# Kernel tuning notes

Measured on AMD Instinct MI355X. Metric: run time of the kernel, lower is better.

## Reference

```python
import jax, jax.numpy as jnp
import numpy as np

B, S, D = 2, 4096, 768
H = 12
HD = D // H  # 64


def setup_inputs() -> dict:
    key = jax.random.key(0)
    ks = jax.random.split(key, 5)
    scale = 1.0 / np.sqrt(D)
    x = jax.random.normal(ks[0], (B, S, D), dtype=jnp.float32)
    Wq = jax.random.normal(ks[1], (D, D), dtype=jnp.float32) * scale
    Wk = jax.random.normal(ks[2], (D, D), dtype=jnp.float32) * scale
    Wv = jax.random.normal(ks[3], (D, D), dtype=jnp.float32) * scale
    Wo = jax.random.normal(ks[4], (D, D), dtype=jnp.float32) * scale
    zb = jnp.zeros((D,), dtype=jnp.float32)
    return {"x": x, "Wq": Wq, "bq": zb, "Wk": Wk, "bk": zb, "Wv": Wv, "bv": zb, "Wo": Wo, "bo": zb}


def reference(x, Wq, bq, Wk, bk, Wv, bv, Wo, bo):
    b, s, d = x.shape
    # projections: nn.Linear computes x @ W^T + b; here W is stored as [in, out]-style [D, D]
    def proj(W, bias):
        y = jnp.einsum('bsd,ed->bse', x, W) + bias  # matches torch Linear (weight [out,in])
        return y.reshape(b, s, H, HD).transpose(0, 2, 1, 3)  # [B,H,S,HD]
    q = proj(Wq, bq)
    k = proj(Wk, bk)
    v = proj(Wv, bv)
    att = jnp.einsum('bhqd,bhkd->bhqk', q, k) / np.sqrt(HD).astype(np.float32)
    causal = jnp.tril(jnp.ones((s, s), dtype=bool))
    att = jnp.where(causal, att, -jnp.inf)
    att = jax.nn.softmax(att, axis=-1)  # dropout p=0 (eval)
    y = jnp.einsum('bhqk,bhkd->bhqd', att, v)
    y = y.transpose(0, 2, 1, 3).reshape(b, s, d)
    return jnp.einsum('bsd,ed->bse', y, Wo) + bo
```

## Files before the change

### kernel.cpp

```cpp
#include <hip/hip_runtime.h>
#include <hip/hip_bf16.h>

typedef __bf16 bf16;
typedef __attribute__((ext_vector_type(8))) __bf16 bf16x8;
typedef __attribute__((ext_vector_type(4))) __bf16 bf16x4;
typedef __attribute__((ext_vector_type(4))) float f32x4;
typedef __attribute__((ext_vector_type(16))) float f32x16;

#if __has_builtin(__builtin_amdgcn_permlane32_swap)
#define HAVE_PLSWAP 1
typedef __attribute__((ext_vector_type(2))) unsigned uint2v;
#endif

#define MFMA16(a, b, c) __builtin_amdgcn_mfma_f32_16x16x32_bf16((a), (b), (c), 0, 0, 0)
#define MFMA32(a, b, c) __builtin_amdgcn_mfma_f32_32x32x16_bf16((a), (b), (c), 0, 0, 0)

__device__ __forceinline__ void gload_lds16(const bf16* g, bf16* l) {
  __builtin_amdgcn_global_load_lds(
      (const __attribute__((address_space(1))) void*)g,
      (__attribute__((address_space(3))) void*)l, 16, 0, 0);
}

__device__ __forceinline__ unsigned pkbf(float a, float b) {
  union { unsigned u; bf16 h[2]; } w;
  w.h[0] = (bf16)a; w.h[1] = (bf16)b;
  return w.u;
}

#define CBAR(N)                                               \
  do {                                                        \
    asm volatile("s_waitcnt vmcnt(" #N ") lgkmcnt(0)" ::: "memory"); \
    __builtin_amdgcn_s_barrier();                             \
    __builtin_amdgcn_sched_barrier(0);                        \
  } while (0)

__global__ void cvt_all(const float* __restrict__ x,
                        const float* __restrict__ wq, const float* __restrict__ wk,
                        const float* __restrict__ wv, const float* __restrict__ wo,
                        bf16* __restrict__ xb, bf16* __restrict__ Wb) {
  constexpr int NX4 = 6291456 / 4;
  constexpr int NW4 = 589824 / 4;
  constexpr int TOT = NX4 + 4 * NW4;
  int stride = gridDim.x * blockDim.x;
  for (int i = blockIdx.x * blockDim.x + threadIdx.x; i < TOT; i += stride) {
    const float4* src;
    bf16x4* dst;
    if (i < NX4) {
      src = reinterpret_cast<const float4*>(x) + i;
      dst = reinterpret_cast<bf16x4*>(xb) + i;
    } else {
      int j = i - NX4;
      int w = j / NW4, r = j - w * NW4;
      const float* sp = (w == 0) ? wq : (w == 1) ? wk : (w == 2) ? wv : wo;
      src = reinterpret_cast<const float4*>(sp) + r;
      dst = reinterpret_cast<bf16x4*>(Wb) + j;
    }
    float4 v = *src;
    bf16x4 o = {(bf16)v.x, (bf16)v.y, (bf16)v.z, (bf16)v.w};
    *dst = o;
  }
}

template <bool OUT_BF16>
__global__ __launch_bounds__(256) void gemm_bt(
    const bf16* __restrict__ A, const bf16* __restrict__ W,
    const float* __restrict__ b0, const float* __restrict__ b1, const float* __restrict__ b2,
    float* __restrict__ Cf, bf16* __restrict__ Cb,
    int M, int N, int K) {
  const int z = blockIdx.z;
  const bf16* Wz = W + (size_t)z * N * K;
  const float* bias = (z == 0) ? b0 : (z == 1 ? b1 : b2);

  __shared__ alignas(16) bf16 As[128 * 64];
  __shared__ alignas(16) bf16 Bs[128 * 64];

  const int tid = threadIdx.x;
  const int wave = tid >> 6, lane = tid & 63;
  const int lr = lane & 15, lg = lane >> 4;
  const int wr = wave >> 1, wc = wave & 1;
  const int m0 = blockIdx.y * 128, n0 = blockIdx.x * 128;

  f32x4 acc[4][4] = {};

  for (int k0 = 0; k0 < K; k0 += 64) {
    __syncthreads();
#pragma unroll
    for (int j = 0; j < 4; ++j) {
      int cb = j * 256 + wave * 64;
      int c = cb + lane;
      int row = c >> 3, x = c & 7;
      int xs = x ^ (row & 7);
      gload_lds16(&A[(size_t)(m0 + row) * K + k0 + xs * 8], &As[cb * 8]);
      gload_lds16(&Wz[(size_t)(n0 + row) * K + k0 + xs * 8], &Bs[cb * 8]);
    }
    __syncthreads();
#pragma unroll
    for (int kk = 0; kk < 2; ++kk) {
      bf16x8 af[4], bfr[4];
#pragma unroll
      for (int m = 0; m < 4; ++m) {
        int row = wr * 64 + m * 16 + lr;
        int ch = (kk * 4 + lg) ^ (row & 7);
        af[m] = *reinterpret_cast<const bf16x8*>(&As[row * 64 + ch * 8]);
      }
#pragma unroll
      for (int n = 0; n < 4; ++n) {
        int row = wc * 64 + n * 16 + lr;
        int ch = (kk * 4 + lg) ^ (row & 7);
        bfr[n] = *reinterpret_cast<const bf16x8*>(&Bs[row * 64 + ch * 8]);
      }
      __builtin_amdgcn_s_setprio(1);
#pragma unroll
      for (int m = 0; m < 4; ++m)
#pragma unroll
        for (int n = 0; n < 4; ++n)
          acc[m][n] = MFMA16(af[m], bfr[n], acc[m][n]);
      __builtin_amdgcn_s_setprio(0);
    }
  }

#pragma unroll
  for (int m = 0; m < 4; ++m) {
#pragma unroll
    for (int n = 0; n < 4; ++n) {
#pragma unroll
      for (int i = 0; i < 4; ++i) {
        int row = m0 + wr * 64 + m * 16 + lg * 4 + i;
        int col = n0 + wc * 64 + n * 16 + lr;
        float v = acc[m][n][i] + bias[col];
        if constexpr (OUT_BF16)
          (Cb + (size_t)z * M * N)[(size_t)row * N + col] = (bf16)v;
        else
          Cf[(size_t)row * N + col] = v;
      }
    }
  }
}

__global__ __launch_bounds__(256, 3) void attn32(
    const bf16* __restrict__ Q, const bf16* __restrict__ K,
    const bf16* __restrict__ V, bf16* __restrict__ Y) {
  constexpr int S = 4096, D = 768;
  const int lin = blockIdx.x;
  const int xcd = lin & 7, idx = lin >> 3;
  const int seg = idx >> 5;
  const int pair = xcd * 3 + seg;
  const int jj = idx & 31;
  const int qb = (seg == 0) ? jj
               : (seg == 1) ? ((jj + 16) & 31)
               : (jj < 16 ? 30 - 2 * jj : 63 - 2 * jj);
  const int h = pair % 12, bb = pair / 12;

  const int tid = threadIdx.x, wave = tid >> 6, lane = tid & 63;
  const int ln = lane & 31, hi = lane >> 5;

  const int qw0 = qb * 128 + wave * 32;
  const int qrow = qw0 + ln;
  const int nt = 2 * qb + 2;

  __shared__ alignas(16) bf16 Ks[3][64 * 64];
  __shared__ alignas(16) bf16 Vt[2][64 * 64];

  const size_t head = (size_t)bb * S * D + (size_t)h * 64;
  const float SC2 = 0.125f * 1.44269504089f;

  union U32x4 { unsigned u[4]; bf16x8 v; };
  U32x4 onesU;
  onesU.u[0] = onesU.u[1] = onesU.u[2] = onesU.u[3] = 0x3F803F80u;
  const bf16x8 onesf = onesU.v;

  const f32x16 z16 = {};

  bf16x8 qf[4];
  {
    const bf16* qp = Q + head + (size_t)qrow * D;
#pragma unroll
    for (int c = 0; c < 4; ++c) {
      bf16x8 tq = *reinterpret_cast<const bf16x8*>(qp + c * 16 + hi * 8);
#pragma unroll
      for (int e = 0; e < 8; ++e) tq[e] = (bf16)((float)tq[e] * SC2);
      qf[c] = tq;
    }
  }

  int fOff[4];
#pragma unroll
  for (int i = 0; i < 4; ++i)
    fOff[i] = ln * 64 + ((((2 * i + hi) ^ ln) & 7) * 8);

  const bf16* gk[2];
  int ldsK[2];
#pragma unroll
  for (int j2 = 0; j2 < 2; ++j2) {
    int c = j2 * 256 + tid;
    int r = c >> 3, ch = c & 7;
    gk[j2] = K + head + (size_t)r * D + ((ch ^ (r & 7)) & 7) * 8;
    ldsK[j2] = (j2 * 256 + wave * 64) * 8;
  }

  const int k0v = (tid & 31) * 2, d0 = (tid >> 5) * 8;
  const bf16* gv0 = V + head + (size_t)k0v * D + d0;
  const bf16* gv1 = gv0 + D;
  int wOff[8];
#pragma unroll
  for (int e = 0; e < 8; ++e)
    wOff[e] = (d0 + e) * 64 + ((((k0v >> 3) ^ e) & 7) * 8) + (k0v & 7);

  f32x16 accO0 = {}, accO1 = {}, accL = {};

  auto stageK = [&](int buf) {
#pragma unroll
    for (int j2 = 0; j2 < 2; ++j2) {
      gload_lds16(gk[j2], &Ks[buf][ldsK[j2]]);
      gk[j2] += 64 * D;
    }
  };
  auto loadV = [&](bf16x8* vv) {
    vv[0] = *reinterpret_cast<const bf16x8*>(gv0);
    vv[1] = *reinterpret_cast<const bf16x8*>(gv1);
    gv0 += 64 * D;
    gv1 += 64 * D;
  };
  auto writeV = [&](const bf16x8* vv, int buf) {
#pragma unroll
    for (int e = 0; e < 8; ++e) {
      union { unsigned u; bf16 h[2]; } pw;
      pw.h[0] = vv[0][e]; pw.h[1] = vv[1][e];
      *reinterpret_cast<unsigned*>(&Vt[buf][wOff[e]]) = pw.u;
    }
  };

  {
    bf16x8 v0[2];
    loadV(v0);
    stageK(0);
    stageK(1);
    writeV(v0, 0);
  }
  CBAR(2);

  int curV = 0, curK = 0, sK = 2;
  for (int t = 0; t < nt; ++t) {
    const int kv0 = t * 64;
    const bool more = (t + 1 < nt);
    bf16x8 vnext[2];
    if (more) {
      loadV(vnext);
      if (t + 2 < nt) { stageK(sK); sK = (sK == 2) ? 0 : sK + 1; }
    }

    if (kv0 <= qw0 + 31) {
      const bf16* ksp = &Ks[curK][0];
      f32x16 s0, s1;
      __builtin_amdgcn_s_setprio(1);
      {
        bf16x8 kf0 = *reinterpret_cast<const bf16x8*>(ksp + fOff[0]);
        bf16x8 kf1 = *reinterpret_cast<const bf16x8*>(ksp + fOff[0] + 2048);
        s0 = MFMA32(kf0, qf[0], z16);
        s1 = MFMA32(kf1, qf[0], z16);
      }
#pragma unroll
      for (int c = 1; c < 4; ++c) {
        bf16x8 kf0 = *reinterpret_cast<const bf16x8*>(ksp + fOff[c]);
        bf16x8 kf1 = *reinterpret_cast<const bf16x8*>(ksp + fOff[c] + 2048);
        s0 = MFMA32(kf0, qf[c], s0);
        s1 = MFMA32(kf1, qf[c], s1);
      }
      __builtin_amdgcn_s_setprio(0);

      if (kv0 + 63 > qw0) {
#pragma unroll
        for (int r = 0; r < 16; ++r) {
          int kl = (r & 3) + 8 * (r >> 2) + 4 * hi;
          if (kv0 + kl > qrow) s0[r] = -1e30f;
          if (kv0 + 32 + kl > qrow) s1[r] = -1e30f;
        }
      }

      float p[32];
#pragma unroll
      for (int r = 0; r < 16; ++r) {
        p[r] = __builtin_amdgcn_exp2f(s0[r]);
        p[16 + r] = __builtin_amdgcn_exp2f(s1[r]);
      }

      const bf16* vtp = &Vt[curV][0];
      __builtin_amdgcn_s_setprio(1);
#pragma unroll
      for (int kg = 0; kg < 2; ++kg) {
        const float* pv = &p[kg * 16];
        unsigned w0 = pkbf(pv[0], pv[1]), w1 = pkbf(pv[2], pv[3]);
        unsigned w2 = pkbf(pv[4], pv[5]), w3 = pkbf(pv[6], pv[7]);
        unsigned w4 = pkbf(pv[8], pv[9]), w5 = pkbf(pv[10], pv[11]);
        unsigned w6 = pkbf(pv[12], pv[13]), w7 = pkbf(pv[14], pv[15]);
        union { unsigned u[4]; bf16x8 v; } fe, fo;
#if HAVE_PLSWAP
        uint2v r02 = __builtin_amdgcn_permlane32_swap(w0, w2, false, false);
        uint2v r13 = __builtin_amdgcn_permlane32_swap(w1, w3, false, false);
        uint2v r46 = __builtin_amdgcn_permlane32_swap(w4, w6, false, false);
        uint2v r57 = __builtin_amdgcn_permlane32_swap(w5, w7, false, false);
        fe.u[0] = r02.x; fe.u[1] = r13.x; fe.u[2] = r02.y; fe.u[3] = r13.y;
        fo.u[0] = r46.x; fo.u[1] = r57.x; fo.u[2] = r46.y; fo.u[3] = r57.y;
#else
        unsigned X0 = hi ? w0 : w2, X1 = hi ? w1 : w3;
        unsigned X2 = hi ? w4 : w6, X3 = hi ? w5 : w7;
        unsigned Y0 = __shfl_xor((int)X0, 32), Y1 = __shfl_xor((int)X1, 32);
        unsigned Y2 = __shfl_xor((int)X2, 32), Y3 = __shfl_xor((int)X3, 32);
        fe.u[0] = hi ? Y0 : w0; fe.u[1] = hi ? Y1 : w1;
        fe.u[2] = hi ? w2 : Y0; fe.u[3] = hi ? w3 : Y1;
        fo.u[0] = hi ? Y2 : w4; fo.u[1] = hi ? Y3 : w5;
        fo.u[2] = hi ? w6 : Y2; fo.u[3] = hi ? w7 : Y3;
#endif
#pragma unroll
        for (int half = 0; half < 2; ++half) {
          int kc = 2 * kg + half;
          bf16x8 pf = half ? fo.v : fe.v;
          bf16x8 vf0 = *reinterpret_cast<const bf16x8*>(vtp + fOff[kc]);
          bf16x8 vf1 = *reinterpret_cast<const bf16x8*>(vtp + fOff[kc] + 2048);
          accO0 = MFMA32(vf0, pf, accO0);
          accO1 = MFMA32(vf1, pf, accO1);
          accL = MFMA32(onesf, pf, accL);
        }
      }
      __builtin_amdgcn_s_setprio(0);
    }

    if (more) {
      writeV(vnext, curV ^ 1);
      CBAR(2);
      curV ^= 1;
      curK = (curK == 2) ? 0 : curK + 1;
    }
  }

  float inv = 1.f / accL[0];
  bf16* yp = Y + head + (size_t)qrow * D;
#pragma unroll
  for (int g = 0; g < 4; ++g) {
    bf16x4 o0, o1;
#pragma unroll
    for (int i = 0; i < 4; ++i) {
      o0[i] = (bf16)(accO0[g * 4 + i] * inv);
      o1[i] = (bf16)(accO1[g * 4 + i] * inv);
    }
    *reinterpret_cast<bf16x4*>(yp + 8 * g + 4 * hi) = o0;
    *reinterpret_cast<bf16x4*>(yp + 32 + 8 * g + 4 * hi) = o1;
  }
}

extern "C" void kernel_launch(void* const* d_in, const int* in_sizes, int n_in,
                              void* d_out, int out_size, void* d_ws, size_t ws_size,
                              hipStream_t stream) {
  const float* x  = (const float*)d_in[0];
  const float* Wq = (const float*)d_in[1];
  const float* bq = (const float*)d_in[2];
  const float* Wk = (const float*)d_in[3];
  const float* bk = (const float*)d_in[4];
  const float* Wv = (const float*)d_in[5];
  const float* bv = (const float*)d_in[6];
  const float* Wo = (const float*)d_in[7];
  const float* bo = (const float*)d_in[8];
  float* out = (float*)d_out;

  constexpr int Bx = 2, S = 4096, Dd = 768;
  constexpr int M = Bx * S;
  constexpr size_t XB = (size_t)M * Dd;
  constexpr size_t WB = (size_t)Dd * Dd;

  char* ws = (char*)d_ws;
  bf16* xb = (bf16*)ws;
  bf16* Wb = (bf16*)(ws + 2 * XB);
  bf16* Qb = (bf16*)(ws + 2 * XB + 8 * WB);
  bf16* Kb = Qb + XB;
  bf16* Vb = Kb + XB;
  bf16* Yb = Vb + XB;

  cvt_all<<<2048, 256, 0, stream>>>(x, Wq, Wk, Wv, Wo, xb, Wb);

  gemm_bt<true><<<dim3(6, 64, 3), 256, 0, stream>>>(
      xb, Wb, bq, bk, bv, nullptr, Qb, M, Dd, Dd);

  attn32<<<dim3(768), 256, 0, stream>>>(Qb, Kb, Vb, Yb);

  gemm_bt<false><<<dim3(6, 64, 1), 256, 0, stream>>>(
      Yb, Wb + 3 * WB, bo, bo, bo, out, nullptr, M, Dd, Dd);
}
```

Measured before the change: 177.2 us.

## Split causal attention KV range in two halves and merge with combine kernel

```diff
diff --git a/kernel.cpp b/kernel.cpp
--- a/kernel.cpp
+++ b/kernel.cpp
@@ -137,15 +137,19 @@
   }
 }
 
-__global__ __launch_bounds__(256, 3) void attn32(
+__global__ __launch_bounds__(256, 4) void attn32(
     const bf16* __restrict__ Q, const bf16* __restrict__ K,
-    const bf16* __restrict__ V, bf16* __restrict__ Y) {
+    const bf16* __restrict__ V,
+    bf16* __restrict__ Oa, bf16* __restrict__ Ob,
+    float* __restrict__ La, float* __restrict__ Lb) {
   constexpr int S = 4096, D = 768;
   const int lin = blockIdx.x;
   const int xcd = lin & 7, idx = lin >> 3;
-  const int seg = idx >> 5;
+  const int seg = idx >> 6;
   const int pair = xcd * 3 + seg;
-  const int jj = idx & 31;
+  const int rem = idx & 63;
+  const int jj = rem >> 1;
+  const int part = rem & 1;
   const int qb = (seg == 0) ? jj
                : (seg == 1) ? ((jj + 16) & 31)
                : (jj < 16 ? 30 - 2 * jj : 63 - 2 * jj);
@@ -156,7 +160,8 @@
 
   const int qw0 = qb * 128 + wave * 32;
   const int qrow = qw0 + ln;
-  const int nt = 2 * qb + 2;
+  const int ntL = qb + 1;
+  const int t0rows = part * ntL * 64;
 
   __shared__ alignas(16) bf16 Ks[3][64 * 64];
   __shared__ alignas(16) bf16 Vt[2][64 * 64];
@@ -194,12 +199,12 @@
   for (int j2 = 0; j2 < 2; ++j2) {
     int c = j2 * 256 + tid;
     int r = c >> 3, ch = c & 7;
-    gk[j2] = K + head + (size_t)r * D + ((ch ^ (r & 7)) & 7) * 8;
+    gk[j2] = K + head + (size_t)(r + t0rows) * D + ((ch ^ (r & 7)) & 7) * 8;
     ldsK[j2] = (j2 * 256 + wave * 64) * 8;
   }
 
   const int k0v = (tid & 31) * 2, d0 = (tid >> 5) * 8;
-  const bf16* gv0 = V + head + (size_t)k0v * D + d0;
+  const bf16* gv0 = V + head + (size_t)(k0v + t0rows) * D + d0;
   const bf16* gv1 = gv0 + D;
   int wOff[8];
 #pragma unroll
@@ -240,13 +245,13 @@
   CBAR(2);
 
   int curV = 0, curK = 0, sK = 2;
-  for (int t = 0; t < nt; ++t) {
-    const int kv0 = t * 64;
-    const bool more = (t + 1 < nt);
+  for (int t = 0; t < ntL; ++t) {
+    const int kv0 = (part * ntL + t) * 64;
+    const bool more = (t + 1 < ntL);
     bf16x8 vnext[2];
     if (more) {
       loadV(vnext);
-      if (t + 2 < nt) { stageK(sK); sK = (sK == 2) ? 0 : sK + 1; }
+      if (t + 2 < ntL) { stageK(sK); sK = (sK == 2) ? 0 : sK + 1; }
     }
 
     if (kv0 <= qw0 + 31) {
@@ -333,19 +338,40 @@
     }
   }
 
-  float inv = 1.f / accL[0];
-  bf16* yp = Y + head + (size_t)qrow * D;
+  bf16* op = (part ? Ob : Oa) + head + (size_t)qrow * D;
 #pragma unroll
   for (int g = 0; g < 4; ++g) {
     bf16x4 o0, o1;
 #pragma unroll
     for (int i = 0; i < 4; ++i) {
-      o0[i] = (bf16)(accO0[g * 4 + i] * inv);
-      o1[i] = (bf16)(accO1[g * 4 + i] * inv);
-    }
-    *reinterpret_cast<bf16x4*>(yp + 8 * g + 4 * hi) = o0;
-    *reinterpret_cast<bf16x4*>(yp + 32 + 8 * g + 4 * hi) = o1;
-  }
+      o0[i] = (bf16)accO0[g * 4 + i];
+      o1[i] = (bf16)accO1[g * 4 + i];
+    }
+    *reinterpret_cast<bf16x4*>(op + 8 * g + 4 * hi) = o0;
+    *reinterpret_cast<bf16x4*>(op + 32 + 8 * g + 4 * hi) = o1;
+  }
+  (part ? Lb : La)[((bb * 12 + h) << 12) + qrow] = accL[0];
+}
+
+__global__ __launch_bounds__(256) void combine(
+    const bf16* __restrict__ Oa, const bf16* __restrict__ Ob,
+    const float* __restrict__ La, const float* __restrict__ Lb,
+    bf16* __restrict__ Y) {
+  int i = blockIdx.x * blockDim.x + threadIdx.x;
+  if (i >= 786432) return;
+  int e = i * 8;
+  int rowlin = e >> 6;
+  int h = rowlin % 12;
+  int t = rowlin / 12;
+  int s = t & 4095, bb = t >> 12;
+  int lidx = ((bb * 12 + h) << 12) + s;
+  float inv = 1.f / (La[lidx] + Lb[lidx]);
+  bf16x8 a = *reinterpret_cast<const bf16x8*>(Oa + e);
+  bf16x8 b = *reinterpret_cast<const bf16x8*>(Ob + e);
+  bf16x8 o;
+#pragma unroll
+  for (int j = 0; j < 8; ++j) o[j] = (bf16)(((float)a[j] + (float)b[j]) * inv);
+  *reinterpret_cast<bf16x8*>(Y + e) = o;
 }
 
 extern "C" void kernel_launch(void* const* d_in, const int* in_sizes, int n_in,
@@ -374,13 +400,19 @@
   bf16* Kb = Qb + XB;
   bf16* Vb = Kb + XB;
   bf16* Yb = Vb + XB;
+  bf16* Obuf = Yb + XB;
+  float* La = (float*)(Obuf + XB);
+  float* Lb = La + 24 * 4096;
+  bf16* Oa = xb;
 
   cvt_all<<<2048, 256, 0, stream>>>(x, Wq, Wk, Wv, Wo, xb, Wb);
 
   gemm_bt<true><<<dim3(6, 64, 3), 256, 0, stream>>>(
       xb, Wb, bq, bk, bv, nullptr, Qb, M, Dd, Dd);
 
-  attn32<<<dim3(768), 256, 0, stream>>>(Qb, Kb, Vb, Yb);
+  attn32<<<dim3(1536), 256, 0, stream>>>(Qb, Kb, Vb, Oa, Obuf, La, Lb);
+
+  combine<<<dim3(3072), 256, 0, stream>>>(Oa, Obuf, La, Lb, Yb);
 
   gemm_bt<false><<<dim3(6, 64, 1), 256, 0, stream>>>(
       Yb, Wb + 3 * WB, bo, bo, bo, out, nullptr, M, Dd, Dd);
```

After: 189.3 us. 1.07x slower.
